# Performance work log

Hardware: AMD Instinct MI355X
Metric: run time of the kernel (lower is better)

Reference implementation:

```python
import jax, jax.numpy as jnp
import numpy as np

N = 100000
E = 1600000
IN_C, HID, OUT_C = 128, 128, 64
NUM_LAYERS = 3


def setup_inputs() -> dict:
    key = jax.random.key(0)
    ks = jax.random.split(key, 8)
    x = jax.random.normal(ks[0], (N, IN_C), dtype=jnp.float32)
    edge_index = jax.random.randint(ks[1], (2, E), 0, N, dtype=jnp.int64)
    s_in = 1.0 / np.sqrt(IN_C)
    s_h = 1.0 / np.sqrt(HID)
    W_in = jax.random.uniform(ks[2], (IN_C, HID), jnp.float32, -s_in, s_in)
    b_in = jax.random.uniform(ks[3], (HID,), jnp.float32, -s_in, s_in)
    conv_W = jax.random.uniform(ks[4], (NUM_LAYERS, HID, HID), jnp.float32, -s_h, s_h)
    conv_b = jnp.zeros((NUM_LAYERS, HID), jnp.float32)
    W_out = jax.random.uniform(ks[5], (HID, OUT_C), jnp.float32, -s_h, s_h)
    b_out = jax.random.uniform(ks[6], (OUT_C,), jnp.float32, -s_h, s_h)
    return {"x": x, "edge_index": edge_index, "W_in": W_in, "b_in": b_in,
            "conv_W": conv_W, "conv_b": conv_b, "W_out": W_out, "b_out": b_out}


def reference(x, edge_index, W_in, b_in, conv_W, conv_b, W_out, b_out):
    n = x.shape[0]
    loops = jnp.arange(n, dtype=edge_index.dtype)
    # add self-loops (PyG GCNConv default)
    rows = jnp.concatenate([edge_index[0], loops])  # source nodes
    cols = jnp.concatenate([edge_index[1], loops])  # target nodes
    deg = jax.ops.segment_sum(jnp.ones_like(cols, dtype=x.dtype), cols, num_segments=n)
    dinv = jnp.where(deg > 0, jax.lax.rsqrt(deg), 0.0)
    norm = (dinv[rows] * dinv[cols])[:, None]  # [E+N, 1] symmetric normalization

    def gcn_conv(h, W, b):
        h = h @ W  # [N, HID]
        msg = h[rows] * norm  # gather + scale, [E+N, HID]
        return jax.ops.segment_sum(msg, cols, num_segments=n) + b

    h = jax.nn.relu(x @ W_in + b_in)
    for l in range(conv_W.shape[0]):
        h = jax.nn.relu(gcn_conv(h, conv_W[l], conv_b[l]))
    logits = h @ W_out + b_out
    return logits
```

## Files before the change

kernel.cpp:

```cpp
#include <hip/hip_runtime.h>

typedef __attribute__((ext_vector_type(8))) short short8;
typedef __attribute__((ext_vector_type(4))) float f32x4;

#define NPB   128
#define CAPB  2688
#define TILE  4096
#define MAXB  800

__device__ __forceinline__ float bfLO(unsigned u){
  union { unsigned x; float f; } c; c.x = u << 16; return c.f;
}
__device__ __forceinline__ float bfHI(unsigned u){
  union { unsigned x; float f; } c; c.x = u & 0xffff0000u; return c.f;
}
__device__ __forceinline__ unsigned short f2bf(float f){
  union { float f; unsigned u; } v; v.f = f;
  unsigned r = v.u + 0x7fffu + ((v.u >> 16) & 1u);
  return (unsigned short)(r >> 16);
}

__global__ void k_wprep_all(const float* __restrict__ W_in, const float* __restrict__ convW,
                            const float* __restrict__ W_out, unsigned short* __restrict__ Bf,
                            int* __restrict__ zeroPtr, int zeroN){
  if (blockIdx.x >= 40){
    int i = (blockIdx.x - 40)*256 + threadIdx.x;
    if (i < zeroN) zeroPtr[i] = 0;
    return;
  }
  const int slot = blockIdx.x >> 3;
  const int idx  = (blockIdx.x & 7)*256 + threadIdx.x;
  const float* W; int ncol;
  if (slot == 0){ W = W_in; ncol = 128; }
  else if (slot <= 3){ W = convW + (size_t)(slot-1)*128*128; ncol = 128; }
  else { W = W_out; ncol = 64; }
  const int l = idx & 63, ks = (idx >> 6) & 3, cb = idx >> 8;
  if (cb >= (ncol >> 4)) return;
  const int c  = cb*16 + (l & 15);
  const int k0 = ks*32 + ((l >> 4) << 3);
  unsigned short* o = Bf + (size_t)slot*16384 + (size_t)idx*8;
#pragma unroll
  for (int j = 0; j < 8; ++j) o[j] = f2bf(W[(size_t)(k0 + j)*ncol + c]);
}

template<int NCOL, bool A_F32, bool BIAS, bool RELU, bool OUT_F32>
__device__ __forceinline__ void mm_body(int bid, const void* __restrict__ Ap,
    const unsigned short* __restrict__ Bf, const float* __restrict__ bias,
    void* __restrict__ Cp, int nrows)
{
  constexpr int NCB = NCOL/16;
  const int tid = threadIdx.x;
  const int wave = tid >> 6, l = tid & 63;
  const int lr = l & 15, lg = l >> 4;
  const int row0 = bid*128 + wave*32;

  f32x4 acc[2][NCB];
#pragma unroll
  for (int i = 0; i < 2; ++i)
#pragma unroll
    for (int j = 0; j < NCB; ++j) acc[i][j] = f32x4{0.f, 0.f, 0.f, 0.f};

  const int r0 = row0 + lr, r1 = row0 + 16 + lr;
  const bool ok0 = r0 < nrows, ok1 = r1 < nrows;

#pragma unroll
  for (int ks = 0; ks < 4; ++ks){
    const int kbase = ks*32 + lg*8;
    short8 a0 = short8{0,0,0,0,0,0,0,0}, a1 = short8{0,0,0,0,0,0,0,0};
    if constexpr (A_F32){
      const float* A = (const float*)Ap;
      if (ok0){
        const float* p = A + (size_t)r0*128 + kbase;
        f32x4 x0 = *(const f32x4*)p, x1 = *(const f32x4*)(p + 4);
#pragma unroll
        for (int j = 0; j < 4; ++j){ a0[j] = (short)f2bf(x0[j]); a0[j+4] = (short)f2bf(x1[j]); }
      }
      if (ok1){
        const float* p = A + (size_t)r1*128 + kbase;
        f32x4 x0 = *(const f32x4*)p, x1 = *(const f32x4*)(p + 4);
#pragma unroll
        for (int j = 0; j < 4; ++j){ a1[j] = (short)f2bf(x0[j]); a1[j+4] = (short)f2bf(x1[j]); }
      }
    } else {
      const unsigned short* A = (const unsigned short*)Ap;
      if (ok0) a0 = *(const short8*)(A + (size_t)r0*128 + kbase);
      if (ok1) a1 = *(const short8*)(A + (size_t)r1*128 + kbase);
    }
#pragma unroll
    for (int cb = 0; cb < NCB; ++cb){
      short8 b = *(const short8*)(Bf + ((size_t)(cb*4 + ks)*64 + l)*8);
      acc[0][cb] = __builtin_amdgcn_mfma_f32_16x16x32_bf16(a0, b, acc[0][cb], 0, 0, 0);
      acc[1][cb] = __builtin_amdgcn_mfma_f32_16x16x32_bf16(a1, b, acc[1][cb], 0, 0, 0);
    }
  }

#pragma unroll
  for (int rb = 0; rb < 2; ++rb){
#pragma unroll
    for (int j = 0; j < 4; ++j){
      const int r = row0 + rb*16 + lg*4 + j;
      if (r >= nrows) continue;
#pragma unroll
      for (int cb = 0; cb < NCB; ++cb){
        const int c = cb*16 + lr;
        float v = acc[rb][cb][j];
        if constexpr (BIAS) v += bias[c];
        if constexpr (RELU) v = fmaxf(v, 0.0f);
        if constexpr (OUT_F32) ((float*)Cp)[(size_t)r*NCOL + c] = v;
        else ((unsigned short*)Cp)[(size_t)r*NCOL + c] = f2bf(v);
      }
    }
  }
}

template<int NCOL, bool A_F32, bool BIAS, bool RELU, bool OUT_F32>
__global__ __launch_bounds__(256) void k_mm_g(const void* __restrict__ Ap,
    const unsigned short* __restrict__ Bf, const float* __restrict__ bias,
    void* __restrict__ Cp, int nrows){
  mm_body<NCOL, A_F32, BIAS, RELU, OUT_F32>(blockIdx.x, Ap, Bf, bias, Cp, nrows);
}

__device__ __forceinline__ void bucket2_body(int bid, const void* ei,
    int* __restrict__ bcnt, unsigned* __restrict__ buf, int E, int nbuck)
{
  __shared__ unsigned recs[TILE];
  __shared__ unsigned short recb[TILE];
  __shared__ int cnt[MAXB];
  __shared__ int offs[MAXB];
  __shared__ int ofc[MAXB];
  __shared__ int gbase[MAXB];
  __shared__ int sc[256];
  __shared__ int s_i64;

  const int tid = threadIdx.x;
  if (tid < 64){
    unsigned v = ((const unsigned*)ei)[2*tid + 1];
    unsigned long long any = __ballot(v != 0u);
    if (tid == 0) s_i64 = (any == 0ull) ? 1 : 0;
  }
  const int e0 = bid * TILE;
  const int m = min(TILE, E - e0);
  if (m <= 0) return;

  for (int i = tid; i < nbuck; i += 256) cnt[i] = 0;
  __syncthreads();
  const bool i64 = s_i64 != 0;

  for (int i = tid; i < m; i += 256){
    int c = i64 ? (int)((const long long*)ei)[(size_t)E + e0 + i]
                : ((const int*)ei)[(size_t)E + e0 + i];
    atomicAdd(&cnt[c >> 7], 1);
  }
  __syncthreads();

  int lc[4]; int tsum = 0;
#pragma unroll
  for (int j = 0; j < 4; ++j){
    int b = tid*4 + j;
    lc[j] = (b < nbuck) ? cnt[b] : 0;
    tsum += lc[j];
  }
  sc[tid] = tsum; __syncthreads();
  for (int off = 1; off < 256; off <<= 1){
    int a = (tid >= off) ? sc[tid - off] : 0;
    __syncthreads(); sc[tid] += a; __syncthreads();
  }
  int run = sc[tid] - tsum;
#pragma unroll
  for (int j = 0; j < 4; ++j){
    int b = tid*4 + j;
    if (b < nbuck){
      offs[b] = run; ofc[b] = run;
      gbase[b] = lc[j] ? atomicAdd(&bcnt[b*16], lc[j]) : 0;
    }
    run += lc[j];
  }
  __syncthreads();

  for (int i = tid; i < m; i += 256){
    int r, c;
    if (i64){ const long long* p = (const long long*)ei; r = (int)p[e0+i]; c = (int)p[(size_t)E+e0+i]; }
    else    { const int* p = (const int*)ei;            r = p[e0+i];      c = p[(size_t)E+e0+i]; }
    int b = c >> 7;
    int pos = atomicAdd(&ofc[b], 1);
    recs[pos] = ((unsigned)(c & (NPB-1)) << 17) | (unsigned)r;
    recb[pos] = (unsigned short)b;
  }
  __syncthreads();

  for (int i = tid; i < m; i += 256){
    int b = recb[i];
    int dst = gbase[b] + (i - offs[b]);
    if (dst < CAPB) buf[(size_t)b*CAPB + dst] = recs[i];
  }
}

__device__ __forceinline__ void csr2_body(int b, const int* __restrict__ bcnt,
    const unsigned* __restrict__ buf, int2* __restrict__ nspan,
    int* __restrict__ srcl, float* __restrict__ dinv, int* __restrict__ cursor, int N)
{
  __shared__ unsigned recs[CAPB];
  __shared__ int cnt[NPB];
  __shared__ int ex[NPB];
  __shared__ int sc[256];
  __shared__ int s_base;
  const int tid = threadIdx.x;
  const int m = min(bcnt[b*16], CAPB);
  if (tid == 0) s_base = atomicAdd(cursor, m);

  if (tid < NPB) cnt[tid] = 0;
  __syncthreads();
  for (int i = tid; i < m; i += 256){
    unsigned rec = buf[(size_t)b*CAPB + i];
    recs[i] = rec;
    atomicAdd(&cnt[rec >> 17], 1);
  }
  __syncthreads();
  const int base = s_base;
  int v = (tid < NPB) ? cnt[tid] : 0;
  sc[tid] = v; __syncthreads();
  for (int off = 1; off < 256; off <<= 1){
    int a = (tid >= off) ? sc[tid - off] : 0;
    __syncthreads();
    sc[tid] += a;
    __syncthreads();
  }
  if (tid < NPB){
    int excl = sc[tid] - v;
    ex[tid] = excl;
    int g = b*NPB + tid;
    if (g < N){
      nspan[g] = make_int2(base + excl, v);
      dinv[g]  = rsqrtf((float)v + 1.0f);
    }
  }
  __syncthreads();
  for (int i = tid; i < m; i += 256){
    unsigned rec = recs[i];
    int pos = base + atomicAdd(&ex[rec >> 17], 1);
    srcl[pos] = (int)(rec & 0x1FFFFu);
  }
}

__global__ __launch_bounds__(256, 4) void k_fat1(const float* __restrict__ x,
    const unsigned short* __restrict__ Bf, const float* __restrict__ b_in,
    unsigned short* __restrict__ h, const void* ei, int* __restrict__ bcnt,
    unsigned* __restrict__ bbuf, int E, int nbuck, int N, int MB)
{
  if ((int)blockIdx.x < MB)
    mm_body<128, true, true, true, false>(blockIdx.x, x, Bf, b_in, h, N);
  else
    bucket2_body(blockIdx.x - MB, ei, bcnt, bbuf, E, nbuck);
}

__global__ __launch_bounds__(256, 4) void k_fat2(const unsigned short* __restrict__ h,
    const unsigned short* __restrict__ Bf1, unsigned short* __restrict__ t,
    const int* __restrict__ bcnt, const unsigned* __restrict__ bbuf,
    int2* __restrict__ nspan, int* __restrict__ srcl, float* __restrict__ dinv,
    int* __restrict__ cursor, int N, int MB)
{
  if ((int)blockIdx.x < MB)
    mm_body<128, false, false, false, false>(blockIdx.x, h, Bf1, nullptr, t, N);
  else
    csr2_body(blockIdx.x - MB, bcnt, bbuf, nspan, srcl, dinv, cursor, N);
}

template<bool SCALED, bool HNEXT>
__global__ __launch_bounds__(256, 8) void k_agg(const unsigned* __restrict__ t,
    const int2* __restrict__ nspan, const int* __restrict__ srcl,
    const float* __restrict__ dinv, const float* __restrict__ bias,
    unsigned* __restrict__ hout, int n)
{
  const int node = blockIdx.x*4 + (threadIdx.x >> 6);
  if (node >= n) return;
  const int l = threadIdx.x & 63;

  const int2 sp = nspan[node];
  int i = sp.x;
  const int e = sp.x + sp.y;
  const float dvc = dinv[node];

  unsigned v = t[(size_t)node*64 + l];
  float a0, a1;
  if constexpr (SCALED){ a0 = dvc*bfLO(v); a1 = dvc*bfHI(v); }
  else                 { a0 = bfLO(v);     a1 = bfHI(v); }

  if constexpr (SCALED){
    int idx = (i < e) ? srcl[min(i + l, e - 1)] : 0;
    while (i < e){
      const int cnt = min(e - i, 64);
      const int nexti = i + cnt;
      const int idxn = (nexti < e) ? srcl[min(nexti + l, e - 1)] : 0;
      int j = 0;
      for (; j + 8 <= cnt; j += 8){
        int sv[8]; unsigned u[8]; float dv[8];
#pragma unroll
        for (int q = 0; q < 8; ++q) sv[q] = __shfl(idx, j + q);
#pragma unroll
        for (int q = 0; q < 8; ++q){ u[q] = t[(size_t)sv[q]*64 + l]; dv[q] = dinv[sv[q]]; }
#pragma unroll
        for (int q = 0; q < 8; ++q){
          a0 = fmaf(dv[q], bfLO(u[q]), a0);
          a1 = fmaf(dv[q], bfHI(u[q]), a1);
        }
      }
      for (; j + 4 <= cnt; j += 4){
        int sv[4]; unsigned u[4]; float dv[4];
#pragma unroll
        for (int q = 0; q < 4; ++q) sv[q] = __shfl(idx, j + q);
#pragma unroll
        for (int q = 0; q < 4; ++q){ u[q] = t[(size_t)sv[q]*64 + l]; dv[q] = dinv[sv[q]]; }
#pragma unroll
        for (int q = 0; q < 4; ++q){
          a0 = fmaf(dv[q], bfLO(u[q]), a0);
          a1 = fmaf(dv[q], bfHI(u[q]), a1);
        }
      }
      for (; j < cnt; ++j){
        int s = __shfl(idx, j);
        unsigned u0 = t[(size_t)s*64 + l];
        float dv0 = dinv[s];
        a0 = fmaf(dv0, bfLO(u0), a0);
        a1 = fmaf(dv0, bfHI(u0), a1);
      }
      i = nexti; idx = idxn;
    }
  } else {
    int idx = (i < e) ? srcl[min(i + l, e - 1)] : 0;
    while (i < e){
      const int cnt = min(e - i, 64);
      const int nexti = i + cnt;
      const int idxn = (nexti < e) ? srcl[min(nexti + l, e - 1)] : 0;
      int j = 0;
      for (; j + 16 <= cnt; j += 16){
        unsigned u[16];
#pragma unroll
        for (int q = 0; q < 16; ++q){
          int s = __builtin_amdgcn_readlane(idx, j + q);
          u[q] = t[(size_t)s*64 + l];
        }
#pragma unroll
        for (int q = 0; q < 16; ++q){ a0 += bfLO(u[q]); a1 += bfHI(u[q]); }
      }
      for (; j + 8 <= cnt; j += 8){
        unsigned u[8];
#pragma unroll
        for (int q = 0; q < 8; ++q){
          int s = __builtin_amdgcn_readlane(idx, j + q);
          u[q] = t[(size_t)s*64 + l];
        }
#pragma unroll
        for (int q = 0; q < 8; ++q){ a0 += bfLO(u[q]); a1 += bfHI(u[q]); }
      }
      for (; j + 4 <= cnt; j += 4){
        unsigned u[4];
#pragma unroll
        for (int q = 0; q < 4; ++q){
          int s = __builtin_amdgcn_readlane(idx, j + q);
          u[q] = t[(size_t)s*64 + l];
        }
#pragma unroll
        for (int q = 0; q < 4; ++q){ a0 += bfLO(u[q]); a1 += bfHI(u[q]); }
      }
      for (; j < cnt; ++j){
        int s = __builtin_amdgcn_readlane(idx, j);
        unsigned u0 = t[(size_t)s*64 + l];
        a0 += bfLO(u0); a1 += bfHI(u0);
      }
      i = nexti; idx = idxn;
    }
  }

  float o0 = fmaxf(fmaf(dvc, a0, bias[2*l]),     0.0f);
  float o1 = fmaxf(fmaf(dvc, a1, bias[2*l + 1]), 0.0f);
  if constexpr (HNEXT){ o0 *= dvc; o1 *= dvc; }
  hout[(size_t)node*64 + l] = (unsigned)f2bf(o0) | ((unsigned)f2bf(o1) << 16);
}

extern "C" void kernel_launch(void* const* d_in, const int* in_sizes, int n_in,
                              void* d_out, int out_size, void* d_ws, size_t ws_size,
                              hipStream_t stream)
{
  const float* x     = (const float*)d_in[0];
  const void*  ei    = d_in[1];
  const float* W_in  = (const float*)d_in[2];
  const float* b_in  = (const float*)d_in[3];
  const float* convW = (const float*)d_in[4];
  const float* convb = (const float*)d_in[5];
  const float* W_out = (const float*)d_in[6];
  const float* b_out = (const float*)d_in[7];
  float* out = (float*)d_out;

  const int N = in_sizes[0] / 128;
  const int E = in_sizes[1] / 2;
  const int NBUCK = (N + NPB - 1) / NPB;

  char* w = (char*)d_ws;
  auto alloc = [&](size_t b){ char* p = w; w += (b + 255) & ~(size_t)255; return p; };
  unsigned short* h    = (unsigned short*)alloc((size_t)N*128*2);
  unsigned short* t    = (unsigned short*)alloc((size_t)N*128*2);
  unsigned short* Bf   = (unsigned short*)alloc((size_t)5*16384*2);
  float* dinv          = (float*)alloc((size_t)N*4);
  int2* nspan          = (int2*)alloc((size_t)N*8);
  int* srcl            = (int*)alloc((size_t)E*4);
  int* bcnt            = (int*)alloc((size_t)(NBUCK*16 + 16)*4);
  unsigned* bbuf       = (unsigned*)d_out;

  int* cursor = bcnt + NBUCK*16;
  const int zeroN = NBUCK*16 + 16;
  const int ZB = (zeroN + 255)/256;
  const int MB = (N + 127) / 128;
  const int NB2 = (E + TILE - 1)/TILE;

  k_wprep_all<<<40 + ZB, 256, 0, stream>>>(W_in, convW, W_out, Bf, bcnt, zeroN);
  k_fat1<<<MB + NB2, 256, 0, stream>>>(x, Bf, b_in, h, ei, bcnt, bbuf, E, NBUCK, N, MB);
  k_fat2<<<MB + NBUCK, 256, 0, stream>>>(h, Bf + (size_t)1*16384, t, bcnt, bbuf,
                                         nspan, srcl, dinv, cursor, N, MB);
  k_agg<true, true><<<(N + 3)/4, 256, 0, stream>>>((const unsigned*)t, nspan, srcl, dinv,
                                                   convb + 0*128, (unsigned*)h, N);
  k_mm_g<128, false, false, false, false><<<MB, 256, 0, stream>>>(h, Bf + (size_t)2*16384, nullptr, t, N);
  k_agg<false, true><<<(N + 3)/4, 256, 0, stream>>>((const unsigned*)t, nspan, srcl, dinv,
                                                    convb + 1*128, (unsigned*)h, N);
  k_mm_g<128, false, false, false, false><<<MB, 256, 0, stream>>>(h, Bf + (size_t)3*16384, nullptr, t, N);
  k_agg<false, false><<<(N + 3)/4, 256, 0, stream>>>((const unsigned*)t, nspan, srcl, dinv,
                                                     convb + 2*128, (unsigned*)h, N);
  k_mm_g<64, false, true, false, true><<<MB, 256, 0, stream>>>(h, Bf + (size_t)4*16384, b_out, out, N);
}
```

Before: 309.6 us.

## Store transformed features in column-blocked layout and aggregate per feature-slice

The matmul now writes its bf16 output in four column blocks of 32 features (node-major within each block). The aggregation kernel assigns each block of 256 threads to one feature slice, with 16 lanes per node and 4 nodes per wave. Each lane reads the neighbour indices directly instead of broadcasting them across a 64-lane wave. The goal is a smaller working set per gather pass, which should improve cache hit rates, plus less lane idling on low-degree nodes. The edge-bucketing step is split out of the fused first kernel into its own launch, and TILE is doubled. These changes add launches and redundant index loads, one per slice.

```diff
diff --git a/kernel.cpp b/kernel.cpp
--- a/kernel.cpp
+++ b/kernel.cpp
@@ -5,7 +5,7 @@
 
 #define NPB   128
 #define CAPB  2688
-#define TILE  4096
+#define TILE  8192
 #define MAXB  800
 
 __device__ __forceinline__ float bfLO(unsigned u){
@@ -43,7 +43,7 @@
   for (int j = 0; j < 8; ++j) o[j] = f2bf(W[(size_t)(k0 + j)*ncol + c]);
 }
 
-template<int NCOL, bool A_F32, bool BIAS, bool RELU, bool OUT_F32>
+template<int NCOL, bool A_F32, bool BIAS, bool RELU, bool OUT_F32, bool TBLK4>
 __device__ __forceinline__ void mm_body(int bid, const void* __restrict__ Ap,
     const unsigned short* __restrict__ Bf, const float* __restrict__ bias,
     void* __restrict__ Cp, int nrows)
@@ -107,20 +107,22 @@
         if constexpr (BIAS) v += bias[c];
         if constexpr (RELU) v = fmaxf(v, 0.0f);
         if constexpr (OUT_F32) ((float*)Cp)[(size_t)r*NCOL + c] = v;
+        else if constexpr (TBLK4)
+          ((unsigned short*)Cp)[((size_t)(c >> 5)*nrows + r)*32 + (c & 31)] = f2bf(v);
         else ((unsigned short*)Cp)[(size_t)r*NCOL + c] = f2bf(v);
       }
     }
   }
 }
 
-template<int NCOL, bool A_F32, bool BIAS, bool RELU, bool OUT_F32>
+template<int NCOL, bool A_F32, bool BIAS, bool RELU, bool OUT_F32, bool TBLK4>
 __global__ __launch_bounds__(256) void k_mm_g(const void* __restrict__ Ap,
     const unsigned short* __restrict__ Bf, const float* __restrict__ bias,
     void* __restrict__ Cp, int nrows){
-  mm_body<NCOL, A_F32, BIAS, RELU, OUT_F32>(blockIdx.x, Ap, Bf, bias, Cp, nrows);
-}
-
-__device__ __forceinline__ void bucket2_body(int bid, const void* ei,
+  mm_body<NCOL, A_F32, BIAS, RELU, OUT_F32, TBLK4>(blockIdx.x, Ap, Bf, bias, Cp, nrows);
+}
+
+__global__ __launch_bounds__(256) void k_bucket2(const void* ei,
     int* __restrict__ bcnt, unsigned* __restrict__ buf, int E, int nbuck)
 {
   __shared__ unsigned recs[TILE];
@@ -138,7 +140,7 @@
     unsigned long long any = __ballot(v != 0u);
     if (tid == 0) s_i64 = (any == 0ull) ? 1 : 0;
   }
-  const int e0 = bid * TILE;
+  const int e0 = blockIdx.x * TILE;
   const int m = min(TILE, E - e0);
   if (m <= 0) return;
 
@@ -242,17 +244,6 @@
   }
 }
 
-__global__ __launch_bounds__(256, 4) void k_fat1(const float* __restrict__ x,
-    const unsigned short* __restrict__ Bf, const float* __restrict__ b_in,
-    unsigned short* __restrict__ h, const void* ei, int* __restrict__ bcnt,
-    unsigned* __restrict__ bbuf, int E, int nbuck, int N, int MB)
-{
-  if ((int)blockIdx.x < MB)
-    mm_body<128, true, true, true, false>(blockIdx.x, x, Bf, b_in, h, N);
-  else
-    bucket2_body(blockIdx.x - MB, ei, bcnt, bbuf, E, nbuck);
-}
-
 __global__ __launch_bounds__(256, 4) void k_fat2(const unsigned short* __restrict__ h,
     const unsigned short* __restrict__ Bf1, unsigned short* __restrict__ t,
     const int* __restrict__ bcnt, const unsigned* __restrict__ bbuf,
@@ -260,121 +251,100 @@
     int* __restrict__ cursor, int N, int MB)
 {
   if ((int)blockIdx.x < MB)
-    mm_body<128, false, false, false, false>(blockIdx.x, h, Bf1, nullptr, t, N);
+    mm_body<128, false, false, false, false, true>(blockIdx.x, h, Bf1, nullptr, t, N);
   else
     csr2_body(blockIdx.x - MB, bcnt, bbuf, nspan, srcl, dinv, cursor, N);
 }
 
 template<bool SCALED, bool HNEXT>
-__global__ __launch_bounds__(256, 8) void k_agg(const unsigned* __restrict__ t,
+__global__ __launch_bounds__(256, 8) void k_agg4(const unsigned* __restrict__ t4,
     const int2* __restrict__ nspan, const int* __restrict__ srcl,
     const float* __restrict__ dinv, const float* __restrict__ bias,
     unsigned* __restrict__ hout, int n)
 {
-  const int node = blockIdx.x*4 + (threadIdx.x >> 6);
+  const int g  = blockIdx.x & 3;
+  const int nb = blockIdx.x >> 2;
+  const int tid = threadIdx.x, wv = tid >> 6, l = tid & 63;
+  const int es = l >> 4, fl = l & 15;
+  const float b0 = bias[g*32 + 2*fl], b1 = bias[g*32 + 2*fl + 1];
+  const int node = nb*16 + wv*4 + es;
   if (node >= n) return;
-  const int l = threadIdx.x & 63;
+  const unsigned* tg = t4 + (size_t)g*n*16;
 
   const int2 sp = nspan[node];
-  int i = sp.x;
-  const int e = sp.x + sp.y;
+  const int i0 = sp.x, deg = sp.y;
   const float dvc = dinv[node];
 
-  unsigned v = t[(size_t)node*64 + l];
+  unsigned v = tg[(size_t)node*16 + fl];
   float a0, a1;
   if constexpr (SCALED){ a0 = dvc*bfLO(v); a1 = dvc*bfHI(v); }
   else                 { a0 = bfLO(v);     a1 = bfHI(v); }
 
+  int i = 0;
   if constexpr (SCALED){
-    int idx = (i < e) ? srcl[min(i + l, e - 1)] : 0;
-    while (i < e){
-      const int cnt = min(e - i, 64);
-      const int nexti = i + cnt;
-      const int idxn = (nexti < e) ? srcl[min(nexti + l, e - 1)] : 0;
-      int j = 0;
-      for (; j + 8 <= cnt; j += 8){
-        int sv[8]; unsigned u[8]; float dv[8];
-#pragma unroll
-        for (int q = 0; q < 8; ++q) sv[q] = __shfl(idx, j + q);
-#pragma unroll
-        for (int q = 0; q < 8; ++q){ u[q] = t[(size_t)sv[q]*64 + l]; dv[q] = dinv[sv[q]]; }
-#pragma unroll
-        for (int q = 0; q < 8; ++q){
-          a0 = fmaf(dv[q], bfLO(u[q]), a0);
-          a1 = fmaf(dv[q], bfHI(u[q]), a1);
-        }
-      }
-      for (; j + 4 <= cnt; j += 4){
-        int sv[4]; unsigned u[4]; float dv[4];
-#pragma unroll
-        for (int q = 0; q < 4; ++q) sv[q] = __shfl(idx, j + q);
-#pragma unroll
-        for (int q = 0; q < 4; ++q){ u[q] = t[(size_t)sv[q]*64 + l]; dv[q] = dinv[sv[q]]; }
-#pragma unroll
-        for (int q = 0; q < 4; ++q){
-          a0 = fmaf(dv[q], bfLO(u[q]), a0);
-          a1 = fmaf(dv[q], bfHI(u[q]), a1);
-        }
-      }
-      for (; j < cnt; ++j){
-        int s = __shfl(idx, j);
-        unsigned u0 = t[(size_t)s*64 + l];
-        float dv0 = dinv[s];
-        a0 = fmaf(dv0, bfLO(u0), a0);
-        a1 = fmaf(dv0, bfHI(u0), a1);
-      }
-      i = nexti; idx = idxn;
+    for (; i + 8 <= deg; i += 8){
+      unsigned sx[8], u[8]; float dv[8];
+#pragma unroll
+      for (int q = 0; q < 8; ++q) sx[q] = (unsigned)srcl[i0 + i + q];
+#pragma unroll
+      for (int q = 0; q < 8; ++q) u[q] = tg[(size_t)sx[q]*16 + fl];
+#pragma unroll
+      for (int q = 0; q < 8; ++q) dv[q] = dinv[sx[q]];
+#pragma unroll
+      for (int q = 0; q < 8; ++q){
+        a0 = fmaf(dv[q], bfLO(u[q]), a0);
+        a1 = fmaf(dv[q], bfHI(u[q]), a1);
+      }
+    }
+    if (i < deg){
+#pragma unroll
+      for (int q = 0; q < 8; ++q){
+        int off = max(min(i + q, deg - 1), 0);
+        unsigned sx = (unsigned)srcl[i0 + off] & 0x1FFFFu;
+        unsigned u = tg[(size_t)sx*16 + fl];
+        float m = (i + q < deg) ? 1.0f : 0.0f;
+        float dv = m * dinv[sx];
+        a0 = fmaf(dv, bfLO(u), a0);
+        a1 = fmaf(dv, bfHI(u), a1);
+      }
     }
   } else {
-    int idx = (i < e) ? srcl[min(i + l, e - 1)] : 0;
-    while (i < e){
-      const int cnt = min(e - i, 64);
-      const int nexti = i + cnt;
-      const int idxn = (nexti < e) ? srcl[min(nexti + l, e - 1)] : 0;
-      int j = 0;
-      for (; j + 16 <= cnt; j += 16){
-        unsigned u[16];
-#pragma unroll
-        for (int q = 0; q < 16; ++q){
-          int s = __builtin_amdgcn_readlane(idx, j + q);
-          u[q] = t[(size_t)s*64 + l];
-        }
-#pragma unroll
-        for (int q = 0; q < 16; ++q){ a0 += bfLO(u[q]); a1 += bfHI(u[q]); }
-      }
-      for (; j + 8 <= cnt; j += 8){
-        unsigned u[8];
-#pragma unroll
-        for (int q = 0; q < 8; ++q){
-          int s = __builtin_amdgcn_readlane(idx, j + q);
-          u[q] = t[(size_t)s*64 + l];
-        }
-#pragma unroll
-        for (int q = 0; q < 8; ++q){ a0 += bfLO(u[q]); a1 += bfHI(u[q]); }
-      }
-      for (; j + 4 <= cnt; j += 4){
-        unsigned u[4];
-#pragma unroll
-        for (int q = 0; q < 4; ++q){
-          int s = __builtin_amdgcn_readlane(idx, j + q);
-          u[q] = t[(size_t)s*64 + l];
-        }
-#pragma unroll
-        for (int q = 0; q < 4; ++q){ a0 += bfLO(u[q]); a1 += bfHI(u[q]); }
-      }
-      for (; j < cnt; ++j){
-        int s = __builtin_amdgcn_readlane(idx, j);
-        unsigned u0 = t[(size_t)s*64 + l];
-        a0 += bfLO(u0); a1 += bfHI(u0);
-      }
-      i = nexti; idx = idxn;
-    }
-  }
-
-  float o0 = fmaxf(fmaf(dvc, a0, bias[2*l]),     0.0f);
-  float o1 = fmaxf(fmaf(dvc, a1, bias[2*l + 1]), 0.0f);
+    for (; i + 16 <= deg; i += 16){
+      unsigned sx[16], u[16];
+#pragma unroll
+      for (int q = 0; q < 16; ++q) sx[q] = (unsigned)srcl[i0 + i + q];
+#pragma unroll
+      for (int q = 0; q < 16; ++q) u[q] = tg[(size_t)sx[q]*16 + fl];
+#pragma unroll
+      for (int q = 0; q < 16; ++q){ a0 += bfLO(u[q]); a1 += bfHI(u[q]); }
+    }
+    if (i + 8 <= deg){
+      unsigned sx[8], u[8];
+#pragma unroll
+      for (int q = 0; q < 8; ++q) sx[q] = (unsigned)srcl[i0 + i + q];
+#pragma unroll
+      for (int q = 0; q < 8; ++q) u[q] = tg[(size_t)sx[q]*16 + fl];
+#pragma unroll
+      for (int q = 0; q < 8; ++q){ a0 += bfLO(u[q]); a1 += bfHI(u[q]); }
+      i += 8;
+    }
+    if (i < deg){
+#pragma unroll
+      for (int q = 0; q < 8; ++q){
+        int off = max(min(i + q, deg - 1), 0);
+        unsigned sx = (unsigned)srcl[i0 + off] & 0x1FFFFu;
+        unsigned u = tg[(size_t)sx*16 + fl];
+        float m = (i + q < deg) ? 1.0f : 0.0f;
+        a0 = fmaf(m, bfLO(u), a0);
+        a1 = fmaf(m, bfHI(u), a1);
+      }
+    }
+  }
+
+  float o0 = fmaxf(fmaf(dvc, a0, b0), 0.0f);
+  float o1 = fmaxf(fmaf(dvc, a1, b1), 0.0f);
   if constexpr (HNEXT){ o0 *= dvc; o1 *= dvc; }
-  hout[(size_t)node*64 + l] = (unsigned)f2bf(o0) | ((unsigned)f2bf(o1) << 16);
+  hout[(size_t)node*64 + g*16 + fl] = (unsigned)f2bf(o0) | ((unsigned)f2bf(o1) << 16);
 }
 
 extern "C" void kernel_launch(void* const* d_in, const int* in_sizes, int n_in,
@@ -398,11 +368,11 @@
   char* w = (char*)d_ws;
   auto alloc = [&](size_t b){ char* p = w; w += (b + 255) & ~(size_t)255; return p; };
   unsigned short* h    = (unsigned short*)alloc((size_t)N*128*2);
-  unsigned short* t    = (unsigned short*)alloc((size_t)N*128*2);
+  unsigned short* t    = (unsigned short*)alloc((size_t)N*128*2 + (1u<<22));
   unsigned short* Bf   = (unsigned short*)alloc((size_t)5*16384*2);
   float* dinv          = (float*)alloc((size_t)N*4);
   int2* nspan          = (int2*)alloc((size_t)N*8);
-  int* srcl            = (int*)alloc((size_t)E*4);
+  int* srcl            = (int*)alloc((size_t)E*4 + 256);
   int* bcnt            = (int*)alloc((size_t)(NBUCK*16 + 16)*4);
   unsigned* bbuf       = (unsigned*)d_out;
 
@@ -411,18 +381,20 @@
   const int ZB = (zeroN + 255)/256;
   const int MB = (N + 127) / 128;
   const int NB2 = (E + TILE - 1)/TILE;
+  const int AGB = 4*((N + 15)/16);
 
   k_wprep_all<<<40 + ZB, 256, 0, stream>>>(W_in, convW, W_out, Bf, bcnt, zeroN);
-  k_fat1<<<MB + NB2, 256, 0, stream>>>(x, Bf, b_in, h, ei, bcnt, bbuf, E, NBUCK, N, MB);
+  k_bucket2<<<NB2, 256, 0, stream>>>(ei, bcnt, bbuf, E, NBUCK);
+  k_mm_g<128, true, true, true, false, false><<<MB, 256, 0, stream>>>(x, Bf, b_in, h, N);
   k_fat2<<<MB + NBUCK, 256, 0, stream>>>(h, Bf + (size_t)1*16384, t, bcnt, bbuf,
                                          nspan, srcl, dinv, cursor, N, MB);
-  k_agg<true, true><<<(N + 3)/4, 256, 0, stream>>>((const unsigned*)t, nspan, srcl, dinv,
-                                                   convb + 0*128, (unsigned*)h, N);
-  k_mm_g<128, false, false, false, false><<<MB, 256, 0, stream>>>(h, Bf + (size_t)2*16384, nullptr, t, N);
-  k_agg<false, true><<<(N + 3)/4, 256, 0, stream>>>((const unsigned*)t, nspan, srcl, dinv,
-                                                    convb + 1*128, (unsigned*)h, N);
-  k_mm_g<128, false, false, false, false><<<MB, 256, 0, stream>>>(h, Bf + (size_t)3*16384, nullptr, t, N);
-  k_agg<false, false><<<(N + 3)/4, 256, 0, stream>>>((const unsigned*)t, nspan, srcl, dinv,
-                                                     convb + 2*128, (unsigned*)h, N);
-  k_mm_g<64, false, true, false, true><<<MB, 256, 0, stream>>>(h, Bf + (size_t)4*16384, b_out, out, N);
-}
+  k_agg4<true, true><<<AGB, 256, 0, stream>>>((const unsigned*)t, nspan, srcl, dinv,
+                                              convb + 0*128, (unsigned*)h, N);
+  k_mm_g<128, false, false, false, false, true><<<MB, 256, 0, stream>>>(h, Bf + (size_t)2*16384, nullptr, t, N);
+  k_agg4<false, true><<<AGB, 256, 0, stream>>>((const unsigned*)t, nspan, srcl, dinv,
+                                               convb + 1*128, (unsigned*)h, N);
+  k_mm_g<128, false, false, false, false, true><<<MB, 256, 0, stream>>>(h, Bf + (size_t)3*16384, nullptr, t, N);
+  k_agg4<false, false><<<AGB, 256, 0, stream>>>((const unsigned*)t, nspan, srcl, dinv,
+                                                convb + 2*128, (unsigned*)h, N);
+  k_mm_g<64, false, true, false, true, false><<<MB, 256, 0, stream>>>(h, Bf + (size_t)4*16384, b_out, out, N);
+}
```

After: 363.5 us. 1.17x slower.
